# Kernel optimization log

Measured on AMD Instinct MI355X. Metric: run time of the kernel, lower is better.

Reference implementation:

```python
import jax, jax.numpy as jnp
import numpy as np

N_NODES = 50000
N_EDGES = 500000
IN_F, HID, EMB = 128, 256, 128

def setup_inputs() -> dict:
    key = jax.random.key(0)
    ks = jax.random.split(key, 9)
    x = jax.random.normal(ks[0], (N_NODES, IN_F), dtype=jnp.float32)
    src = jax.random.randint(ks[1], (N_EDGES,), 0, N_NODES, dtype=jnp.int32)
    dst = jax.random.randint(ks[2], (N_EDGES,), 0, N_NODES, dtype=jnp.int32)
    def lin(k, fan_in, fan_out):
        bound = 1.0 / np.sqrt(fan_in)
        kw, kb = jax.random.split(k)
        W = jax.random.uniform(kw, (fan_in, fan_out), minval=-bound, maxval=bound, dtype=jnp.float32)
        b = jax.random.uniform(kb, (fan_out,), minval=-bound, maxval=bound, dtype=jnp.float32)
        return W, b
    W1, b1 = lin(ks[3], IN_F, HID)
    W2, b2 = lin(ks[4], HID, HID)
    W3, b3 = lin(ks[5], HID, EMB)
    return {"x": x, "src": src, "dst": dst, "W1": W1, "b1": b1,
            "W2": W2, "b2": b2, "W3": W3, "b3": b3}

def _gcn_layer(h, src, dst, W, b):
    # sum messages from src nodes into dst nodes, then linear
    agg = jax.ops.segment_sum(h[src], dst, num_segments=N_NODES)  # [N, F]
    return agg @ W + b

def reference(x, src, dst, W1, b1, W2, b2, W3, b3):
    h = jax.nn.relu(_gcn_layer(x, src, dst, W1, b1))
    h = jax.nn.relu(_gcn_layer(h, src, dst, W2, b2))
    h = _gcn_layer(h, src, dst, W3, b3)
    # dgl.mean_nodes on a single graph: mean of relu(h) over all nodes -> [EMB]
    return jnp.mean(jax.nn.relu(h), axis=0)
```

## Files before the change

kernel.cpp:

```cpp
#include <hip/hip_runtime.h>

#define N_NODES 50000
#define N_EDGES 500000

typedef __attribute__((ext_vector_type(8))) short short8;
typedef __attribute__((ext_vector_type(8))) unsigned short ushort8v;
typedef __attribute__((ext_vector_type(4))) float floatx4;
typedef __attribute__((ext_vector_type(4))) unsigned int uint4v;

__device__ inline float bf2f(unsigned short u) {
    unsigned int x = ((unsigned int)u) << 16;
    return __builtin_bit_cast(float, x);
}
__device__ inline unsigned short f2bf(float f) {
    unsigned int x = __builtin_bit_cast(unsigned int, f);
    x += 0x7fff + ((x >> 16) & 1);
    return (unsigned short)(x >> 16);
}

__device__ __forceinline__ void gld_lds16(const unsigned short* g, unsigned short* l) {
    __builtin_amdgcn_global_load_lds((const __attribute__((address_space(1))) void*)g,
                                     (__attribute__((address_space(3))) void*)l, 16, 0, 0);
}

__device__ inline void accum16B(float2* a, ushort8v rv) {
    uint4v u = __builtin_bit_cast(uint4v, rv);
    #pragma unroll
    for (int p = 0; p < 4; p++) {
        float lo = __builtin_bit_cast(float, u[p] << 16);
        float hi = __builtin_bit_cast(float, u[p] & 0xFFFF0000u);
        a[p].x += lo;
        a[p].y += hi;
    }
}


__global__ __launch_bounds__(256) void histprep_kernel(const int* __restrict__ dst,
                                                       int* __restrict__ deg,
                                                       const float* __restrict__ W1,
                                                       const float* __restrict__ W2,
                                                       const float* __restrict__ W3,
                                                       const float* __restrict__ x,
                                                       unsigned short* __restrict__ Wt1,
                                                       unsigned short* __restrict__ Wt2,
                                                       unsigned short* __restrict__ Wt3,
                                                       unsigned short* __restrict__ xb,
                                                       int* __restrict__ bsum,
                                                       float* __restrict__ outZ) {
    int idx = blockIdx.x * 256 + threadIdx.x;
    if (idx < N_EDGES) { atomicAdd(&deg[dst[idx]], 1); return; }
    idx -= N_EDGES;
    if (idx < 32768) {
        if (idx < 256) bsum[idx] = 0;
        if (idx < 128) outZ[idx] = 0.f;
        int k = idx >> 8, n = idx & 255;
        Wt1[n * 128 + k] = f2bf(W1[idx]);
    } else if (idx < 98304) {
        int i = idx - 32768;
        int k = i >> 8, n = i & 255;
        Wt2[n * 256 + k] = f2bf(W2[i]);
    } else if (idx < 131072) {
        int i = idx - 98304;
        int k = i >> 7, n = i & 127;
        Wt3[n * 256 + k] = f2bf(W3[i]);
    } else {
        int i = (idx - 131072) * 4;
        if (i < N_NODES * 128) {
            float4 v = *(const float4*)(x + i);
            ushort4 o;
            o.x = f2bf(v.x); o.y = f2bf(v.y); o.z = f2bf(v.z); o.w = f2bf(v.w);
            *(ushort4*)(xb + i) = o;
        }
    }
}


__global__ __launch_bounds__(256) void scan_onepass_kernel(int* __restrict__ cur,
                                                           int* __restrict__ bsum,
                                                           int* __restrict__ off, int n) {
    __shared__ int s[256];
    int b = blockIdx.x, t = threadIdx.x;
    int i = b * 256 + t;
    int v = (i < n) ? cur[i] : 0;
    s[t] = v;
    __syncthreads();
    #pragma unroll
    for (int d = 1; d < 256; d <<= 1) {
        int u = (t >= d) ? s[t - d] : 0;
        __syncthreads();
        s[t] += u;
        __syncthreads();
    }
    int incl = s[t];
    if (t == 255) atomicExch(&bsum[b], s[255] + 1);
    int pre = 0;
    if (t < b) {
        volatile int* p = (volatile int*)&bsum[t];
        int vv;
        while ((vv = *p) == 0) { }
        pre = vv - 1;
    }
    __syncthreads();
    s[t] = pre;
    __syncthreads();
    #pragma unroll
    for (int d = 128; d > 0; d >>= 1) {
        if (t < d) s[t] += s[t + d];
        __syncthreads();
    }
    int base = s[0];
    if (i == 0) off[0] = 0;
    if (i < n) {
        int inclG = base + incl;
        off[i + 1] = inclG;
        cur[i] = inclG - v;
    }
}

__global__ void fill_kernel(const int* __restrict__ src, const int* __restrict__ dst,
                            int* __restrict__ cur, int* __restrict__ csr, int nE) {
    int e = blockIdx.x * 256 + threadIdx.x;
    if (e < nE) {
        int p = atomicAdd(&cur[dst[e]], 1);
        csr[p] = src[e];
    }
}


__global__ __launch_bounds__(256) void agg256_kernel(const unsigned short* __restrict__ h,
                                                     const int* __restrict__ off,
                                                     const int* __restrict__ csr,
                                                     unsigned short* __restrict__ outp) {
    int wave = threadIdx.x >> 6, lane = threadIdx.x & 63;
    int node = blockIdx.x * 4 + wave;
    int half = lane >> 5;
    int f0 = (lane & 31) * 8;
    int s = __builtin_amdgcn_readfirstlane(off[node]);
    int e = __builtin_amdgcn_readfirstlane(off[node + 1]);
    float2 a[4];
    #pragma unroll
    for (int p = 0; p < 4; p++) a[p] = make_float2(0.f, 0.f);
    int i = s;
    for (; i + 8 <= e; i += 8) {
        ushort8v r[4];
        #pragma unroll
        for (int j = 0; j < 4; j++) {
            int i0 = csr[i + 2 * j];
            int i1 = csr[i + 2 * j + 1];
            int id = half ? i1 : i0;
            r[j] = *(const ushort8v*)(h + (size_t)id * 256 + f0);
        }
        #pragma unroll
        for (int j = 0; j < 4; j++) accum16B(a, r[j]);
    }
    int rem = e - i;
    if (rem > 0) {
        int nr = (rem + 1) >> 1;
        ushort8v r[4];
        #pragma unroll
        for (int j = 0; j < 4; j++) {
            if (j < nr) {
                int b0 = i + 2 * j, b1 = b0 + 1;
                int i0 = csr[b0];
                int i1 = csr[b1 < e ? b1 : e - 1];
                int id = half ? i1 : i0;
                r[j] = *(const ushort8v*)(h + (size_t)id * 256 + f0);
            }
        }
        #pragma unroll
        for (int j = 0; j < 4; j++) {
            if (j < nr && (i + 2 * j + half) < e) accum16B(a, r[j]);
        }
    }
    #pragma unroll
    for (int p = 0; p < 4; p++) {
        a[p].x += __shfl_xor(a[p].x, 32, 64);
        a[p].y += __shfl_xor(a[p].y, 32, 64);
    }
    if (half == 0) {
        ushort8v o;
        #pragma unroll
        for (int p = 0; p < 4; p++) { o[2 * p] = f2bf(a[p].x); o[2 * p + 1] = f2bf(a[p].y); }
        *(ushort8v*)(outp + (size_t)node * 256 + f0) = o;
    }
}


__device__ inline void agg128_body(const unsigned short* __restrict__ h,
                                   const int* __restrict__ off,
                                   const int* __restrict__ csr,
                                   int node, int quad, int f0, float2* a) {
    int s = __builtin_amdgcn_readfirstlane(off[node]);
    int e = __builtin_amdgcn_readfirstlane(off[node + 1]);
    int i = s;
    for (; i + 8 <= e; i += 8) {
        ushort8v r[2];
        #pragma unroll
        for (int j = 0; j < 2; j++) {
            int base = i + 4 * j;
            int i0 = csr[base], i1 = csr[base + 1], i2 = csr[base + 2], i3 = csr[base + 3];
            int id = quad == 0 ? i0 : quad == 1 ? i1 : quad == 2 ? i2 : i3;
            r[j] = *(const ushort8v*)(h + (size_t)id * 128 + f0);
        }
        #pragma unroll
        for (int j = 0; j < 2; j++) accum16B(a, r[j]);
    }
    int rem = e - i;
    if (rem > 0) {
        int nr = (rem + 3) >> 2;
        ushort8v r[2];
        #pragma unroll
        for (int j = 0; j < 2; j++) {
            if (j < nr) {
                int base = i + 4 * j;
                int c1 = base + 1 < e ? base + 1 : e - 1;
                int c2 = base + 2 < e ? base + 2 : e - 1;
                int c3 = base + 3 < e ? base + 3 : e - 1;
                int i0 = csr[base], i1 = csr[c1], i2 = csr[c2], i3 = csr[c3];
                int id = quad == 0 ? i0 : quad == 1 ? i1 : quad == 2 ? i2 : i3;
                r[j] = *(const ushort8v*)(h + (size_t)id * 128 + f0);
            }
        }
        #pragma unroll
        for (int j = 0; j < 2; j++) {
            if (j < nr && (i + 4 * j + quad) < e) accum16B(a, r[j]);
        }
    }
    #pragma unroll
    for (int p = 0; p < 4; p++) {
        a[p].x += __shfl_xor(a[p].x, 16, 64);
        a[p].y += __shfl_xor(a[p].y, 16, 64);
        a[p].x += __shfl_xor(a[p].x, 32, 64);
        a[p].y += __shfl_xor(a[p].y, 32, 64);
    }
}

__global__ __launch_bounds__(256) void agg128_kernel(const unsigned short* __restrict__ h,
                                                     const int* __restrict__ off,
                                                     const int* __restrict__ csr,
                                                     unsigned short* __restrict__ outp) {
    int wave = threadIdx.x >> 6, lane = threadIdx.x & 63;
    int node = blockIdx.x * 4 + wave;
    int quad = lane >> 4;
    int f0 = (lane & 15) * 8;
    float2 a[4];
    #pragma unroll
    for (int p = 0; p < 4; p++) a[p] = make_float2(0.f, 0.f);
    agg128_body(h, off, csr, node, quad, f0, a);
    if (quad == 0) {
        ushort8v o;
        #pragma unroll
        for (int p = 0; p < 4; p++) { o[2 * p] = f2bf(a[p].x); o[2 * p + 1] = f2bf(a[p].y); }
        *(ushort8v*)(outp + (size_t)node * 128 + f0) = o;
    }
}


__global__ __launch_bounds__(256) void agg3_mean_kernel(const unsigned short* __restrict__ t,
                                                        const int* __restrict__ off,
                                                        const int* __restrict__ csr,
                                                        const float* __restrict__ b3,
                                                        float* __restrict__ partial) {
    __shared__ float sm[4 * 128];
    int wave = threadIdx.x >> 6, lane = threadIdx.x & 63;
    int node = blockIdx.x * 4 + wave;
    int quad = lane >> 4;
    int f0 = (lane & 15) * 8;
    float2 a[4];
    #pragma unroll
    for (int p = 0; p < 4; p++) a[p] = make_float2(0.f, 0.f);
    agg128_body(t, off, csr, node, quad, f0, a);
    if (quad == 0) {
        #pragma unroll
        for (int p = 0; p < 4; p++) {
            sm[wave * 128 + f0 + 2 * p]     = fmaxf(a[p].x + b3[f0 + 2 * p], 0.f);
            sm[wave * 128 + f0 + 2 * p + 1] = fmaxf(a[p].y + b3[f0 + 2 * p + 1], 0.f);
        }
    }
    __syncthreads();
    if (threadIdx.x < 128) {
        int f = threadIdx.x;
        float p = sm[f] + sm[128 + f] + sm[256 + f] + sm[384 + f];
        partial[(size_t)blockIdx.x * 128 + f] = p;
    }
}

__global__ __launch_bounds__(256) void mean_reduce_kernel(const float* __restrict__ partial,
                                                          float* __restrict__ outp, int nRows) {
    __shared__ float s[256];
    int f = threadIdx.x & 127, half = threadIdx.x >> 7;
    int chunk = (nRows + gridDim.x - 1) / gridDim.x;
    int r0 = blockIdx.x * chunk;
    int r1 = r0 + chunk < nRows ? r0 + chunk : nRows;
    float acc = 0.f;
    for (int r = r0 + half; r < r1; r += 2) acc += partial[(size_t)r * 128 + f];
    s[threadIdx.x] = acc;
    __syncthreads();
    if (half == 0) atomicAdd(&outp[f], (s[f] + s[f + 128]) * (1.0f / N_NODES));
}


template<typename T> __device__ inline void storeC(T* p, float v);
template<> __device__ inline void storeC<float>(float* p, float v) { *p = v; }
template<> __device__ inline void storeC<unsigned short>(unsigned short* p, float v) { *p = f2bf(v); }

template<typename OUT_T>
__global__ __launch_bounds__(256) void gemm_bf16_kernel(const unsigned short* __restrict__ A,
                                                        const unsigned short* __restrict__ Bt,
                                                        const float* __restrict__ bias,
                                                        OUT_T* __restrict__ C,
                                                        int M, int K, int N, int doRelu) {
    constexpr int BM = 64, BN = 128, BK = 32;
    __shared__ unsigned short As[BM * BK];
    __shared__ unsigned short Bs[BN * BK];
    int tid = threadIdx.x;
    int m0 = blockIdx.y * BM, n0 = blockIdx.x * BN;
    int wave = tid >> 6, lane = tid & 63;
    int wm = wave >> 1, wn = wave & 1;
    int mlane = lane & 15, kgrp = lane >> 4;

    floatx4 acc[2][4];
    #pragma unroll
    for (int i = 0; i < 2; i++)
        #pragma unroll
        for (int j = 0; j < 4; j++) acc[i][j] = (floatx4){0.f, 0.f, 0.f, 0.f};

    for (int k0 = 0; k0 < K; k0 += BK) {
        {
            int c = tid;
            int r = c >> 2, cb = (c & 3) * 8;
            gld_lds16(A + (size_t)(m0 + r) * K + k0 + cb, &As[c * 8]);
        }
        #pragma unroll
        for (int it = 0; it < 2; it++) {
            int c = tid + it * 256;
            int r = c >> 2, cb = (c & 3) * 8;
            gld_lds16(Bt + (size_t)(n0 + r) * K + k0 + cb, &Bs[c * 8]);
        }
        __syncthreads();
        short8 af[2], bfr[4];
        #pragma unroll
        for (int mt = 0; mt < 2; mt++)
            af[mt] = *(const short8*)&As[(wm * 32 + mt * 16 + mlane) * BK + kgrp * 8];
        #pragma unroll
        for (int nt = 0; nt < 4; nt++)
            bfr[nt] = *(const short8*)&Bs[(wn * 64 + nt * 16 + mlane) * BK + kgrp * 8];
        #pragma unroll
        for (int mt = 0; mt < 2; mt++)
            #pragma unroll
            for (int nt = 0; nt < 4; nt++)
                acc[mt][nt] = __builtin_amdgcn_mfma_f32_16x16x32_bf16(af[mt], bfr[nt],
                                                                      acc[mt][nt], 0, 0, 0);
        __syncthreads();
    }
    #pragma unroll
    for (int mt = 0; mt < 2; mt++) {
        #pragma unroll
        for (int nt = 0; nt < 4; nt++) {
            int col = n0 + wn * 64 + nt * 16 + mlane;
            float bv = bias ? bias[col] : 0.f;
            #pragma unroll
            for (int r = 0; r < 4; r++) {
                int row = m0 + wm * 32 + mt * 16 + kgrp * 4 + r;
                if (row < M) {
                    float v = acc[mt][nt][r] + bv;
                    if (doRelu) v = fmaxf(v, 0.f);
                    storeC(C + (size_t)row * N + col, v);
                }
            }
        }
    }
}


extern "C" void kernel_launch(void* const* d_in, const int* in_sizes, int n_in,
                              void* d_out, int out_size, void* d_ws, size_t ws_size,
                              hipStream_t stream) {
    const float* x   = (const float*)d_in[0];
    const int*   src = (const int*)d_in[1];
    const int*   dst = (const int*)d_in[2];
    const float* W1 = (const float*)d_in[3];
    const float* b1 = (const float*)d_in[4];
    const float* W2 = (const float*)d_in[5];
    const float* b2 = (const float*)d_in[6];
    const float* W3 = (const float*)d_in[7];
    const float* b3 = (const float*)d_in[8];
    float* out = (float*)d_out;

    char* ws = (char*)d_ws;
    size_t o = 0;
    auto alloc = [&](size_t bytes) -> char* {
        char* p = ws + o;
        o = (o + bytes + 255) & ~(size_t)255;
        return p;
    };
    int* off     = (int*)alloc((size_t)(N_NODES + 1) * 4);
    int* cur     = (int*)alloc((size_t)N_NODES * 4);
    int* csrIdx  = (int*)alloc((size_t)N_EDGES * 4);
    int* bsum    = (int*)alloc(256 * 4);
    unsigned short* Wt1 = (unsigned short*)alloc((size_t)128 * 256 * 2);
    unsigned short* Wt2 = (unsigned short*)alloc((size_t)256 * 256 * 2);
    unsigned short* Wt3 = (unsigned short*)alloc((size_t)256 * 128 * 2);
    char* R1 = alloc((size_t)N_NODES * 256 * 2);
    char* R2 = alloc((size_t)N_NODES * 256 * 2);
    char* R3 = alloc((size_t)N_NODES * 256 * 2);
    (void)alloc(65536);

    unsigned short* xb    = (unsigned short*)R1;
    unsigned short* aggX  = (unsigned short*)R2;
    unsigned short* h1    = (unsigned short*)R3;
    unsigned short* agg2o = (unsigned short*)R1;
    unsigned short* h2    = (unsigned short*)R2;
    unsigned short* t     = (unsigned short*)R3;
    float*          pmean = (float*)R1;

    const int nb = (N_NODES + 255) / 256;

    hipMemsetAsync(cur, 0, (size_t)N_NODES * 4, stream);
    const int hpThreads = N_EDGES + 131072 + N_NODES * 128 / 4;
    histprep_kernel<<<(hpThreads + 255) / 256, 256, 0, stream>>>(dst, cur, W1, W2, W3, x,
                                                                 Wt1, Wt2, Wt3, xb, bsum, out);
    scan_onepass_kernel<<<nb, 256, 0, stream>>>(cur, bsum, off, N_NODES);
    fill_kernel<<<(N_EDGES + 255) / 256, 256, 0, stream>>>(src, dst, cur, csrIdx, N_EDGES);

    const int mb = (N_NODES + 63) / 64;

    agg128_kernel<<<N_NODES / 4, 256, 0, stream>>>(xb, off, csrIdx, aggX);
    gemm_bf16_kernel<unsigned short><<<dim3(2, mb), 256, 0, stream>>>(aggX, Wt1, b1, h1,
                                                                      N_NODES, 128, 256, 1);
    agg256_kernel<<<N_NODES / 4, 256, 0, stream>>>(h1, off, csrIdx, agg2o);
    gemm_bf16_kernel<unsigned short><<<dim3(2, mb), 256, 0, stream>>>(agg2o, Wt2, b2, h2,
                                                                      N_NODES, 256, 256, 1);
    gemm_bf16_kernel<unsigned short><<<dim3(1, mb), 256, 0, stream>>>(h2, Wt3, nullptr, t,
                                                                      N_NODES, 256, 128, 0);
    agg3_mean_kernel<<<N_NODES / 4, 256, 0, stream>>>(t, off, csrIdx, b3, pmean);
    mean_reduce_kernel<<<128, 256, 0, stream>>>(pmean, out, N_NODES / 4);
}
```

Baseline: 299.4 us.

## Fuse neighbor aggregation with bf16 GEMM for first two GCN layers

Replaces the separate agg128/agg256 kernels and their follow-up GEMMs with one templated kernel. Each 64-row block gathers and sums neighbor features into LDS, then runs an MFMA GEMM against double-buffered weight tiles and applies bias and ReLU. This drops the write and re-read of the aggregated intermediate in global memory and removes two launches. In exchange, the gather now uses fewer lanes per node with less parallelism and latency hiding, blocks are larger and use more LDS (fewer blocks, 782), and the GEMM cannot start until the whole gather phase finishes.

```diff
diff --git a/kernel.cpp b/kernel.cpp
--- a/kernel.cpp
+++ b/kernel.cpp
@@ -127,61 +127,112 @@
 }
 
 
-__global__ __launch_bounds__(256) void agg256_kernel(const unsigned short* __restrict__ h,
-                                                     const int* __restrict__ off,
-                                                     const int* __restrict__ csr,
-                                                     unsigned short* __restrict__ outp) {
-    int wave = threadIdx.x >> 6, lane = threadIdx.x & 63;
-    int node = blockIdx.x * 4 + wave;
-    int half = lane >> 5;
-    int f0 = (lane & 31) * 8;
-    int s = __builtin_amdgcn_readfirstlane(off[node]);
-    int e = __builtin_amdgcn_readfirstlane(off[node + 1]);
-    float2 a[4];
-    #pragma unroll
-    for (int p = 0; p < 4; p++) a[p] = make_float2(0.f, 0.f);
-    int i = s;
-    for (; i + 8 <= e; i += 8) {
-        ushort8v r[4];
-        #pragma unroll
-        for (int j = 0; j < 4; j++) {
-            int i0 = csr[i + 2 * j];
-            int i1 = csr[i + 2 * j + 1];
-            int id = half ? i1 : i0;
-            r[j] = *(const ushort8v*)(h + (size_t)id * 256 + f0);
-        }
-        #pragma unroll
-        for (int j = 0; j < 4; j++) accum16B(a, r[j]);
-    }
-    int rem = e - i;
-    if (rem > 0) {
-        int nr = (rem + 1) >> 1;
-        ushort8v r[4];
-        #pragma unroll
-        for (int j = 0; j < 4; j++) {
-            if (j < nr) {
-                int b0 = i + 2 * j, b1 = b0 + 1;
-                int i0 = csr[b0];
-                int i1 = csr[b1 < e ? b1 : e - 1];
-                int id = half ? i1 : i0;
-                r[j] = *(const ushort8v*)(h + (size_t)id * 256 + f0);
+template<int F>
+__global__ __launch_bounds__(512) void fused_agg_gemm_kernel(const unsigned short* __restrict__ H,
+                                                             const int* __restrict__ off,
+                                                             const int* __restrict__ csr,
+                                                             const unsigned short* __restrict__ Bt,
+                                                             const float* __restrict__ bias,
+                                                             unsigned short* __restrict__ C,
+                                                             int M) {
+    constexpr int BM = 64, BN = 256, BK = 32, KS = F / BK;
+    constexpr int LDAF = F + 8;
+    constexpr int LPR = F / 8;
+    constexpr int G = 512 / LPR;
+    __shared__ unsigned short Afull[BM * LDAF];
+    __shared__ unsigned short Bs[2][BN * BK];
+    int tid = threadIdx.x;
+    int m0 = blockIdx.x * BM;
+
+    #pragma unroll
+    for (int it = 0; it < 2; it++) {
+        int c = tid + it * 512;
+        int r = c >> 2, cb = (c & 3) * 8;
+        gld_lds16(Bt + (size_t)r * F + cb, &Bs[0][c * 8]);
+    }
+
+    {
+        int gid = tid / LPR, li = tid % LPR;
+        int f0 = li * 8;
+        for (int n = gid; n < BM; n += G) {
+            int node = m0 + n;
+            if (node < M) {
+                int s = off[node], e = off[node + 1];
+                float2 a[4];
+                #pragma unroll
+                for (int p = 0; p < 4; p++) a[p] = make_float2(0.f, 0.f);
+                int i = s;
+                for (; i + 4 <= e; i += 4) {
+                    int i0 = csr[i], i1 = csr[i + 1], i2 = csr[i + 2], i3 = csr[i + 3];
+                    ushort8v r0 = *(const ushort8v*)(H + (size_t)i0 * F + f0);
+                    ushort8v r1 = *(const ushort8v*)(H + (size_t)i1 * F + f0);
+                    ushort8v r2 = *(const ushort8v*)(H + (size_t)i2 * F + f0);
+                    ushort8v r3 = *(const ushort8v*)(H + (size_t)i3 * F + f0);
+                    accum16B(a, r0); accum16B(a, r1); accum16B(a, r2); accum16B(a, r3);
+                }
+                for (; i < e; i++) {
+                    ushort8v r0 = *(const ushort8v*)(H + (size_t)csr[i] * F + f0);
+                    accum16B(a, r0);
+                }
+                ushort8v o;
+                #pragma unroll
+                for (int p = 0; p < 4; p++) { o[2 * p] = f2bf(a[p].x); o[2 * p + 1] = f2bf(a[p].y); }
+                *(ushort8v*)&Afull[n * LDAF + f0] = o;
             }
         }
-        #pragma unroll
-        for (int j = 0; j < 4; j++) {
-            if (j < nr && (i + 2 * j + half) < e) accum16B(a, r[j]);
-        }
-    }
-    #pragma unroll
-    for (int p = 0; p < 4; p++) {
-        a[p].x += __shfl_xor(a[p].x, 32, 64);
-        a[p].y += __shfl_xor(a[p].y, 32, 64);
-    }
-    if (half == 0) {
-        ushort8v o;
-        #pragma unroll
-        for (int p = 0; p < 4; p++) { o[2 * p] = f2bf(a[p].x); o[2 * p + 1] = f2bf(a[p].y); }
-        *(ushort8v*)(outp + (size_t)node * 256 + f0) = o;
+    }
+    __syncthreads();
+
+    int wave = tid >> 6, lane = tid & 63;
+    int wm = wave & 1, wn = wave >> 1;
+    int mlane = lane & 15, kgrp = lane >> 4;
+    floatx4 acc[2][4];
+    #pragma unroll
+    for (int i = 0; i < 2; i++)
+        #pragma unroll
+        for (int j = 0; j < 4; j++) acc[i][j] = (floatx4){0.f, 0.f, 0.f, 0.f};
+
+    for (int ks = 0; ks < KS; ks++) {
+        if (ks + 1 < KS) {
+            int buf = (ks + 1) & 1;
+            #pragma unroll
+            for (int it = 0; it < 2; it++) {
+                int c = tid + it * 512;
+                int r = c >> 2, cb = (c & 3) * 8;
+                gld_lds16(Bt + (size_t)r * F + (ks + 1) * BK + cb, &Bs[buf][c * 8]);
+            }
+        }
+        const unsigned short* bsb = Bs[ks & 1];
+        short8 af[2], bfr[4];
+        #pragma unroll
+        for (int mt = 0; mt < 2; mt++)
+            af[mt] = *(const short8*)&Afull[(wm * 32 + mt * 16 + mlane) * LDAF + ks * BK + kgrp * 8];
+        #pragma unroll
+        for (int nt = 0; nt < 4; nt++)
+            bfr[nt] = *(const short8*)&bsb[(wn * 64 + nt * 16 + mlane) * BK + kgrp * 8];
+        #pragma unroll
+        for (int mt = 0; mt < 2; mt++)
+            #pragma unroll
+            for (int nt = 0; nt < 4; nt++)
+                acc[mt][nt] = __builtin_amdgcn_mfma_f32_16x16x32_bf16(af[mt], bfr[nt],
+                                                                      acc[mt][nt], 0, 0, 0);
+        __syncthreads();
+    }
+    #pragma unroll
+    for (int mt = 0; mt < 2; mt++) {
+        #pragma unroll
+        for (int nt = 0; nt < 4; nt++) {
+            int col = wn * 64 + nt * 16 + mlane;
+            float bv = bias[col];
+            #pragma unroll
+            for (int r = 0; r < 4; r++) {
+                int row = m0 + wm * 32 + mt * 16 + kgrp * 4 + r;
+                if (row < M) {
+                    float v = fmaxf(acc[mt][nt][r] + bv, 0.f);
+                    C[(size_t)row * BN + col] = f2bf(v);
+                }
+            }
+        }
     }
 }
 
@@ -232,26 +283,6 @@
         a[p].y += __shfl_xor(a[p].y, 16, 64);
         a[p].x += __shfl_xor(a[p].x, 32, 64);
         a[p].y += __shfl_xor(a[p].y, 32, 64);
-    }
-}
-
-__global__ __launch_bounds__(256) void agg128_kernel(const unsigned short* __restrict__ h,
-                                                     const int* __restrict__ off,
-                                                     const int* __restrict__ csr,
-                                                     unsigned short* __restrict__ outp) {
-    int wave = threadIdx.x >> 6, lane = threadIdx.x & 63;
-    int node = blockIdx.x * 4 + wave;
-    int quad = lane >> 4;
-    int f0 = (lane & 15) * 8;
-    float2 a[4];
-    #pragma unroll
-    for (int p = 0; p < 4; p++) a[p] = make_float2(0.f, 0.f);
-    agg128_body(h, off, csr, node, quad, f0, a);
-    if (quad == 0) {
-        ushort8v o;
-        #pragma unroll
-        for (int p = 0; p < 4; p++) { o[2 * p] = f2bf(a[p].x); o[2 * p + 1] = f2bf(a[p].y); }
-        *(ushort8v*)(outp + (size_t)node * 128 + f0) = o;
     }
 }
 
@@ -407,9 +438,7 @@
     (void)alloc(65536);
 
     unsigned short* xb    = (unsigned short*)R1;
-    unsigned short* aggX  = (unsigned short*)R2;
     unsigned short* h1    = (unsigned short*)R3;
-    unsigned short* agg2o = (unsigned short*)R1;
     unsigned short* h2    = (unsigned short*)R2;
     unsigned short* t     = (unsigned short*)R3;
     float*          pmean = (float*)R1;
@@ -423,16 +452,12 @@
     scan_onepass_kernel<<<nb, 256, 0, stream>>>(cur, bsum, off, N_NODES);
     fill_kernel<<<(N_EDGES + 255) / 256, 256, 0, stream>>>(src, dst, cur, csrIdx, N_EDGES);
 
-    const int mb = (N_NODES + 63) / 64;
-
-    agg128_kernel<<<N_NODES / 4, 256, 0, stream>>>(xb, off, csrIdx, aggX);
-    gemm_bf16_kernel<unsigned short><<<dim3(2, mb), 256, 0, stream>>>(aggX, Wt1, b1, h1,
-                                                                      N_NODES, 128, 256, 1);
-    agg256_kernel<<<N_NODES / 4, 256, 0, stream>>>(h1, off, csrIdx, agg2o);
-    gemm_bf16_kernel<unsigned short><<<dim3(2, mb), 256, 0, stream>>>(agg2o, Wt2, b2, h2,
-                                                                      N_NODES, 256, 256, 1);
-    gemm_bf16_kernel<unsigned short><<<dim3(1, mb), 256, 0, stream>>>(h2, Wt3, nullptr, t,
-                                                                      N_NODES, 256, 128, 0);
+    const int mbF = (N_NODES + 63) / 64;
+
+    fused_agg_gemm_kernel<128><<<mbF, 512, 0, stream>>>(xb, off, csrIdx, Wt1, b1, h1, N_NODES);
+    fused_agg_gemm_kernel<256><<<mbF, 512, 0, stream>>>(h1, off, csrIdx, Wt2, b2, h2, N_NODES);
+    gemm_bf16_kernel<unsigned short><<<dim3(1, mbF), 256, 0, stream>>>(h2, Wt3, nullptr, t,
+                                                                       N_NODES, 256, 128, 0);
     agg3_mean_kernel<<<N_NODES / 4, 256, 0, stream>>>(t, off, csrIdx, b3, pmean);
     mean_reduce_kernel<<<128, 256, 0, stream>>>(pmean, out, N_NODES / 4);
 }
```

Result: faster. 291.8 us (-2.5%).
